# Optimization experiments

Hardware: AMD Instinct MI355X
Metric: run time of the kernel (lower is better)

Reference implementation:

```python
import jax, jax.numpy as jnp
import numpy as np
from jax import lax

B, CIN, T, H, W_ = 16, 8, 20, 64, 64
COUT = 32
K = 3


def setup_inputs() -> dict:
    key = jax.random.key(0)
    ks = jax.random.split(key, 6)
    scale = 0.05
    return {
        "X": jax.random.normal(ks[0], (B, CIN, T, H, W_), dtype=jnp.float32),
        "W": jax.random.normal(ks[1], (4 * COUT, CIN + COUT, K, K), dtype=jnp.float32) * scale,
        "b": jax.random.normal(ks[2], (4 * COUT,), dtype=jnp.float32) * scale,
        "W_ci": jax.random.normal(ks[3], (COUT, H, W_), dtype=jnp.float32) * scale,
        "W_cf": jax.random.normal(ks[4], (COUT, H, W_), dtype=jnp.float32) * scale,
        "W_co": jax.random.normal(ks[5], (COUT, H, W_), dtype=jnp.float32) * scale,
    }


def reference(X, W, b, W_ci, W_cf, W_co):
    # X: (B, Cin, T, H, W) -> output (B, Cout, T, H, W)
    Bb, Cin, Tt, Hh, Ww = X.shape
    Cout = W_ci.shape[0]

    def conv(x):  # x: (B, Cin+Cout, H, W)
        y = lax.conv_general_dilated(
            x, W, window_strides=(1, 1), padding="SAME",
            dimension_numbers=("NCHW", "OIHW", "NCHW"))
        return y + b[None, :, None, None]

    def step(carry, x_t):
        h, c = carry
        gates = conv(jnp.concatenate([x_t, h], axis=1))  # (B, 4*Cout, H, W)
        i_c, f_c, cc_c, o_c = jnp.split(gates, 4, axis=1)
        i_g = jax.nn.sigmoid(i_c + W_ci[None] * c)
        f_g = jax.nn.sigmoid(f_c + W_cf[None] * c)
        c_new = f_g * c + i_g * jnp.tanh(cc_c)
        o_g = jax.nn.sigmoid(o_c + W_co[None] * c_new)
        h_new = o_g * jnp.tanh(c_new)
        return (h_new, c_new), h_new

    h0 = jnp.zeros((Bb, Cout, Hh, Ww), dtype=X.dtype)
    c0 = jnp.zeros((Bb, Cout, Hh, Ww), dtype=X.dtype)
    x_seq = jnp.moveaxis(X, 2, 0)  # (T, B, Cin, H, W)
    _, hs = lax.scan(step, (h0, c0), x_seq)  # hs: (T, B, Cout, H, W)
    return jnp.moveaxis(hs, 0, 2)  # (B, Cout, T, H, W)
```

## Files before the change

### kernel.cpp

```cpp
#include <hip/hip_runtime.h>
#include <math.h>

#define Bn   16
#define CIN  8
#define NT   20
#define COUT 32
#define HW   4096
#define NTHREADS 256

typedef __attribute__((ext_vector_type(8)))  short bf16x8;
typedef __attribute__((ext_vector_type(16))) float f32x16;
typedef __attribute__((ext_vector_type(4)))  int   int4v;

__device__ inline unsigned short f2bf(float f) {
    unsigned u = __builtin_bit_cast(unsigned, f);
    u += 0x7fffu + ((u >> 16) & 1u);
    return (unsigned short)(u >> 16);
}
__device__ inline float bf2f(unsigned short u) {
    return __builtin_bit_cast(float, (unsigned)u << 16);
}
__device__ inline float sigm(float x) {
    return 1.0f / (1.0f + __expf(-x));
}
__device__ inline float tanh_fast(float x) {
    x = fminf(fmaxf(x, -15.0f), 15.0f);
    float e = __expf(2.0f * x);
    return (e - 1.0f) / (e + 1.0f);
}

__global__ __launch_bounds__(256) void prep_w(const float* __restrict__ W,
                                              unsigned short* __restrict__ Wbf) {
    int idx = blockIdx.x * 256 + threadIdx.x;
    if (idx >= 9 * 3 * 2 * 128 * 8) return;
    int e    = idx & 7;
    int m    = (idx >> 3) & 127;
    int half = (idx >> 10) & 1;
    int fk   = idx >> 11;
    int kb   = fk % 3;
    int tap  = fk / 3;
    int ch   = kb * 16 + half * 8 + e;
    int co   = m >> 2;
    int g    = m & 3;
    float v = 0.0f;
    if (ch < 40) v = W[(size_t)((g * 32 + co) * 40 + ch) * 9 + tap];
    Wbf[idx] = f2bf(v);
}

__global__ __launch_bounds__(256) void zero_flags(int* flags) {
    flags[blockIdx.x * 256 + threadIdx.x] = 0;
}

__global__ __launch_bounds__(NTHREADS, 2) void convlstm_persist(
    const float* __restrict__ X,
    const unsigned short* __restrict__ Wbf,
    const float* __restrict__ bias,
    const float* __restrict__ Wci,
    const float* __restrict__ Wcf,
    const float* __restrict__ Wco,
    float* __restrict__ out,
    unsigned long long* __restrict__ stage,
    int* __restrict__ flags)
{
    __shared__ __align__(16) unsigned char smem[33792 + 24576 + 512];
    unsigned short* Wlds = (unsigned short*)(smem + 33792);
    float*          lds_b = (float*)(smem + 33792 + 24576);

    const int tid = threadIdx.x;
    const int pid = blockIdx.x;
    const int b   = pid >> 5;
    const int TI  = ((pid & 7) << 2) | ((pid >> 3) & 3);
    const int r0  = TI * 2;

    const int wid  = tid >> 6;
    const int lane = tid & 63;
    const int lm   = lane & 31;
    const int half = lane >> 5;

    {
        int4v z = {0, 0, 0, 0};
        for (int i = tid; i < 2112; i += NTHREADS) *(int4v*)(smem + i * 16) = z;
    }
    {
        const float* wsrc[3] = {Wci, Wcf, Wco};
#pragma unroll
        for (int pl = 0; pl < 3; ++pl)
            for (int i = tid; i < 4096; i += NTHREADS) {
                int co = i >> 7, p = i & 127;
                Wlds[pl * 4096 + i] = f2bf(wsrc[pl][(co << 12) + TI * 128 + p]);
            }
        if (tid < 128) lds_b[tid] = bias[tid];
    }

    bf16x8 Af[27];
#pragma unroll
    for (int f = 0; f < 27; ++f)
        Af[f] = *(const bf16x8*)(Wbf + (size_t)((f * 2 + half) * 128 + wid * 32 + lm) * 8);

    float creg[16];
#pragma unroll
    for (int i = 0; i < 16; ++i) creg[i] = 0.0f;

    const unsigned sel0 = half ? 0x01000504u : 0x05040100u;
    const unsigned sel1 = sel0 + 0x02020202u;
    int* myflag = flags + (b << 5) + TI;

    const int  gr  = r0 + wid - 1;
    const bool rok = (unsigned)gr < 64u;
    const float* xbase = X + ((((size_t)b * CIN) * NT) << 12)
                           + (((rok ? gr : 0)) << 6) + lane;
    const size_t chs = (size_t)NT << 12;
    float xr[8];
    if (rok) {
#pragma unroll
        for (int k = 0; k < 8; ++k) xr[k] = xbase[(size_t)k * chs];
    }

    __syncthreads();

    for (int t = 0; t < NT; ++t) {
        const int lcF  = lane + 1;
        const int celF = wid * 33 + (lcF >> 1);
        const int sbF  = (lcF & 1) << 3;
        const int sxF  = (lcF >> 1) & 15;
        if (rok) {
            unsigned d0, d1, d2, d3;
            asm("v_cvt_pk_bf16_f32 %0, %1, %2" : "=v"(d0) : "v"(xr[0]), "v"(xr[1]));
            asm("v_cvt_pk_bf16_f32 %0, %1, %2" : "=v"(d1) : "v"(xr[2]), "v"(xr[3]));
            asm("v_cvt_pk_bf16_f32 %0, %1, %2" : "=v"(d2) : "v"(xr[4]), "v"(xr[5]));
            asm("v_cvt_pk_bf16_f32 %0, %1, %2" : "=v"(d3) : "v"(xr[6]), "v"(xr[7]));
            int4v xq = {(int)d0, (int)d1, (int)d2, (int)d3};
            *(int4v*)(smem + celF * 256 + ((sbF ^ sxF) << 4)) = xq;
        }
        const bool haloL = (wid == 0) && (TI > 0);
        const bool haloR = (wid == 3) && (TI < 31);
        if ((haloL || haloR) && t > 0) {
            if (lane == 0) {
                const int nti = haloL ? TI - 1 : TI + 1;
                const int* fp = flags + (b << 5) + nti;
                while (__hip_atomic_load(fp, __ATOMIC_RELAXED,
                                         __HIP_MEMORY_SCOPE_AGENT) < t)
                    __builtin_amdgcn_s_sleep(1);
            }
            const unsigned long long* sp =
                stage + ((((size_t)((t - 1) & 1) * Bn + b) * 64 + gr) << 9) + lane;
#pragma unroll
            for (int qq = 0; qq < 4; ++qq) {
                unsigned long long v0 = __hip_atomic_load(
                    sp + (2 * qq) * 64, __ATOMIC_RELAXED, __HIP_MEMORY_SCOPE_AGENT);
                unsigned long long v1 = __hip_atomic_load(
                    sp + (2 * qq + 1) * 64, __ATOMIC_RELAXED, __HIP_MEMORY_SCOPE_AGENT);
                const int slot = (sbF | (qq + 1)) ^ sxF;
                int4v hv = {(int)(unsigned)v0, (int)(v0 >> 32),
                            (int)(unsigned)v1, (int)(v1 >> 32)};
                *(int4v*)(smem + celF * 256 + (slot << 4)) = hv;
            }
        }
        __syncthreads();

        if (rok && t + 1 < NT) {
            const float* xp = xbase + ((size_t)(t + 1) << 12);
#pragma unroll
            for (int k = 0; k < 8; ++k) xr[k] = xp[(size_t)k * chs];
        }

        f32x16 acc[4];
#pragma unroll
        for (int nb = 0; nb < 4; ++nb)
#pragma unroll
            for (int r = 0; r < 16; ++r) acc[nb][r] = 0.0f;

        __builtin_amdgcn_s_setprio(1);
#pragma unroll
        for (int dy = 0; dy < 3; ++dy)
#pragma unroll
            for (int dx = 0; dx < 3; ++dx)
#pragma unroll
                for (int kb = 0; kb < 3; ++kb) {
                    const int f    = (dy * 3 + dx) * 3 + kb;
                    const int cidx = kb * 2 + half;
#pragma unroll
                    for (int nb = 0; nb < 4; ++nb) {
                        const int lr   = (nb >> 1) + dy;
                        const int lc   = lm + (nb & 1) * 32 + dx;
                        const int slot = (((lc & 1) << 3) + cidx) ^ ((lc >> 1) & 15);
                        const bf16x8 bf =
                            *(const bf16x8*)(smem + (lr * 33 + (lc >> 1)) * 256 + slot * 16);
                        acc[nb] = __builtin_amdgcn_mfma_f32_32x32x16_bf16(Af[f], bf, acc[nb], 0, 0, 0);
                    }
                }
        __builtin_amdgcn_s_setprio(0);

        __syncthreads();

#pragma unroll
        for (int nb = 0; nb < 4; ++nb) {
            const int p_loc = nb * 32 + lm;
            const int pos   = TI * 128 + p_loc;
            const int col   = (nb & 1) * 32 + lm;
            const int lc    = col + 1;
            const int cell  = (1 + (nb >> 1)) * 33 + (lc >> 1);
            const int sbase = (lc & 1) << 3;
            const int sx    = (lc >> 1) & 15;
            const int row   = r0 + (nb >> 1);
            const bool hstore = (nb >> 1) ? (TI < 31) : (TI > 0);
            float hprev = 0.0f;
#pragma unroll
            for (int j = 0; j < 4; ++j) {
                const int co  = wid * 8 + 2 * j + half;
                const int wof = (co << 7) + p_loc;
                const float c0 = creg[nb * 4 + j];
                const float gi = acc[nb][4 * j + 0] + lds_b[co]      + bf2f(Wlds[wof]) * c0;
                const float gf = acc[nb][4 * j + 1] + lds_b[32 + co] + bf2f(Wlds[4096 + wof]) * c0;
                const float gc = acc[nb][4 * j + 2] + lds_b[64 + co];
                const float gq = acc[nb][4 * j + 3] + lds_b[96 + co];

                const float ig = sigm(gi);
                const float fg = sigm(gf);
                const float cn = fg * c0 + ig * tanh_fast(gc);
                const float og = sigm(gq + bf2f(Wlds[2 * 4096 + wof]) * cn);
                const float hn = og * tanh_fast(cn);

                creg[nb * 4 + j] = cn;
                out[(((size_t)(b * COUT + co) * NT + t) << 12) + pos] = hn;

                if (j & 1) {
                    unsigned pk;
                    asm("v_cvt_pk_bf16_f32 %0, %1, %2" : "=v"(pk) : "v"(hprev), "v"(hn));
                    unsigned other = (unsigned)__shfl_xor((int)pk, 32, 64);
                    unsigned q0 = __builtin_amdgcn_perm(other, pk, sel0);
                    unsigned q1 = __builtin_amdgcn_perm(other, pk, sel1);
                    const int a = j >> 1;
                    if (half == a) {
                        const int q8 = wid * 2 + a;
                        const unsigned long long quad =
                            ((unsigned long long)q1 << 32) | q0;
                        const int tq = 2 + q8;
                        *(unsigned long long*)(smem + cell * 256 +
                            (((sbase | (tq >> 1)) ^ sx) << 4) + ((tq & 1) << 3)) = quad;
                        if (hstore)
                            __hip_atomic_store(
                                stage + ((((size_t)(t & 1) * Bn + b) * 64 + row) << 9)
                                      + (q8 << 6) + col,
                                quad, __ATOMIC_RELAXED, __HIP_MEMORY_SCOPE_AGENT);
                    }
                } else {
                    hprev = hn;
                }
            }
        }

        __syncthreads();
        if (tid == 0)
            __hip_atomic_store(myflag, t + 1, __ATOMIC_RELAXED,
                               __HIP_MEMORY_SCOPE_AGENT);
    }
}

extern "C" void kernel_launch(void* const* d_in, const int* in_sizes, int n_in,
                              void* d_out, int out_size, void* d_ws, size_t ws_size,
                              hipStream_t stream) {
    const float* X    = (const float*)d_in[0];
    const float* Wf   = (const float*)d_in[1];
    const float* bias = (const float*)d_in[2];
    const float* Wci  = (const float*)d_in[3];
    const float* Wcf  = (const float*)d_in[4];
    const float* Wco  = (const float*)d_in[5];
    float* out = (float*)d_out;

    unsigned short*     Wbf   = (unsigned short*)d_ws;
    int*                flags = (int*)((char*)d_ws + 110592);
    unsigned long long* stage = (unsigned long long*)((char*)d_ws + 112640);

    prep_w<<<216, 256, 0, stream>>>(Wf, Wbf);
    zero_flags<<<2, 256, 0, stream>>>(flags);
    convlstm_persist<<<Bn * 32, NTHREADS, 0, stream>>>(
        X, Wbf, bias, Wci, Wcf, Wco, out, stage, flags);
}
```

Before: 357.1 us.

## Fold bias into MFMA weights, stream weight fragments, and drop peephole LDS

The bias becomes a constant-one channel: the unused padded channel 40 at the centre tap holds the bias in the weight matrix, and the LDS halo is pre-filled with bf16 1.0 in that slot, so the bias add leaves the epilogue. The peephole weights are packed into one 64-bit global array per pixel and read directly instead of being staged in LDS. The 27 register-resident A fragments are replaced with per-dy loads from global memory, and the x prefetch is removed. Together these cut LDS and VGPR use so launch bounds can go from 2 to 3 blocks per SM. The cost is repeated global/L2 loads of weights every timestep, and x loads that are no longer hidden behind the MFMA loop.

```diff
diff --git a/kernel.cpp b/kernel.cpp
--- a/kernel.cpp
+++ b/kernel.cpp
@@ -30,6 +30,7 @@
 }
 
 __global__ __launch_bounds__(256) void prep_w(const float* __restrict__ W,
+                                              const float* __restrict__ bias,
                                               unsigned short* __restrict__ Wbf) {
     int idx = blockIdx.x * 256 + threadIdx.x;
     if (idx >= 9 * 3 * 2 * 128 * 8) return;
@@ -43,28 +44,35 @@
     int co   = m >> 2;
     int g    = m & 3;
     float v = 0.0f;
-    if (ch < 40) v = W[(size_t)((g * 32 + co) * 40 + ch) * 9 + tap];
+    if (ch < 40)                     v = W[(size_t)((g * 32 + co) * 40 + ch) * 9 + tap];
+    else if (ch == 40 && tap == 4)   v = bias[g * 32 + co];
     Wbf[idx] = f2bf(v);
+}
+
+__global__ __launch_bounds__(256) void prep_pk(const float* __restrict__ Wci,
+                                               const float* __restrict__ Wcf,
+                                               const float* __restrict__ Wco,
+                                               unsigned long long* __restrict__ Wpk) {
+    int idx = blockIdx.x * 256 + threadIdx.x;
+    unsigned long long v = (unsigned long long)f2bf(Wci[idx])
+                         | ((unsigned long long)f2bf(Wcf[idx]) << 16)
+                         | ((unsigned long long)f2bf(Wco[idx]) << 32);
+    Wpk[idx] = v;
 }
 
 __global__ __launch_bounds__(256) void zero_flags(int* flags) {
     flags[blockIdx.x * 256 + threadIdx.x] = 0;
 }
 
-__global__ __launch_bounds__(NTHREADS, 2) void convlstm_persist(
+__global__ __launch_bounds__(NTHREADS, 3) void convlstm_persist(
     const float* __restrict__ X,
     const unsigned short* __restrict__ Wbf,
-    const float* __restrict__ bias,
-    const float* __restrict__ Wci,
-    const float* __restrict__ Wcf,
-    const float* __restrict__ Wco,
+    const unsigned long long* __restrict__ Wpk,
     float* __restrict__ out,
     unsigned long long* __restrict__ stage,
     int* __restrict__ flags)
 {
-    __shared__ __align__(16) unsigned char smem[33792 + 24576 + 512];
-    unsigned short* Wlds = (unsigned short*)(smem + 33792);
-    float*          lds_b = (float*)(smem + 33792 + 24576);
+    __shared__ __align__(16) unsigned char smem[33792];
 
     const int tid = threadIdx.x;
     const int pid = blockIdx.x;
@@ -77,25 +85,16 @@
     const int lm   = lane & 31;
     const int half = lane >> 5;
 
-    {
-        int4v z = {0, 0, 0, 0};
-        for (int i = tid; i < 2112; i += NTHREADS) *(int4v*)(smem + i * 16) = z;
+    for (int id = tid; id < 2112; id += NTHREADS) {
+        const int cell  = id >> 4;
+        const int slot  = id & 15;
+        const int cp    = (cell % 33) & 15;
+        const int unswz = slot ^ cp;
+        int4v v = {((unswz & 7) == 5) ? 0x3F80 : 0, 0, 0, 0};
+        *(int4v*)(smem + cell * 256 + slot * 16) = v;
     }
-    {
-        const float* wsrc[3] = {Wci, Wcf, Wco};
-#pragma unroll
-        for (int pl = 0; pl < 3; ++pl)
-            for (int i = tid; i < 4096; i += NTHREADS) {
-                int co = i >> 7, p = i & 127;
-                Wlds[pl * 4096 + i] = f2bf(wsrc[pl][(co << 12) + TI * 128 + p]);
-            }
-        if (tid < 128) lds_b[tid] = bias[tid];
-    }
-
-    bf16x8 Af[27];
-#pragma unroll
-    for (int f = 0; f < 27; ++f)
-        Af[f] = *(const bf16x8*)(Wbf + (size_t)((f * 2 + half) * 128 + wid * 32 + lm) * 8);
+
+    const unsigned short* abase = Wbf + (size_t)(half * 128 + wid * 32 + lm) * 8;
 
     float creg[16];
 #pragma unroll
@@ -107,14 +106,6 @@
 
     const int  gr  = r0 + wid - 1;
     const bool rok = (unsigned)gr < 64u;
-    const float* xbase = X + ((((size_t)b * CIN) * NT) << 12)
-                           + (((rok ? gr : 0)) << 6) + lane;
-    const size_t chs = (size_t)NT << 12;
-    float xr[8];
-    if (rok) {
-#pragma unroll
-        for (int k = 0; k < 8; ++k) xr[k] = xbase[(size_t)k * chs];
-    }
 
     __syncthreads();
 
@@ -124,11 +115,15 @@
         const int sbF  = (lcF & 1) << 3;
         const int sxF  = (lcF >> 1) & 15;
         if (rok) {
+            const float* xp = X + ((((size_t)b * CIN) * NT + t) << 12) + (gr << 6) + lane;
+            const size_t chs = (size_t)NT << 12;
+            float x0 = xp[0],       x1 = xp[chs],     x2 = xp[2 * chs], x3 = xp[3 * chs];
+            float x4 = xp[4 * chs], x5 = xp[5 * chs], x6 = xp[6 * chs], x7 = xp[7 * chs];
             unsigned d0, d1, d2, d3;
-            asm("v_cvt_pk_bf16_f32 %0, %1, %2" : "=v"(d0) : "v"(xr[0]), "v"(xr[1]));
-            asm("v_cvt_pk_bf16_f32 %0, %1, %2" : "=v"(d1) : "v"(xr[2]), "v"(xr[3]));
-            asm("v_cvt_pk_bf16_f32 %0, %1, %2" : "=v"(d2) : "v"(xr[4]), "v"(xr[5]));
-            asm("v_cvt_pk_bf16_f32 %0, %1, %2" : "=v"(d3) : "v"(xr[6]), "v"(xr[7]));
+            asm("v_cvt_pk_bf16_f32 %0, %1, %2" : "=v"(d0) : "v"(x0), "v"(x1));
+            asm("v_cvt_pk_bf16_f32 %0, %1, %2" : "=v"(d1) : "v"(x2), "v"(x3));
+            asm("v_cvt_pk_bf16_f32 %0, %1, %2" : "=v"(d2) : "v"(x4), "v"(x5));
+            asm("v_cvt_pk_bf16_f32 %0, %1, %2" : "=v"(d3) : "v"(x6), "v"(x7));
             int4v xq = {(int)d0, (int)d1, (int)d2, (int)d3};
             *(int4v*)(smem + celF * 256 + ((sbF ^ sxF) << 4)) = xq;
         }
@@ -158,12 +153,6 @@
         }
         __syncthreads();
 
-        if (rok && t + 1 < NT) {
-            const float* xp = xbase + ((size_t)(t + 1) << 12);
-#pragma unroll
-            for (int k = 0; k < 8; ++k) xr[k] = xp[(size_t)k * chs];
-        }
-
         f32x16 acc[4];
 #pragma unroll
         for (int nb = 0; nb < 4; ++nb)
@@ -172,12 +161,15 @@
 
         __builtin_amdgcn_s_setprio(1);
 #pragma unroll
-        for (int dy = 0; dy < 3; ++dy)
+        for (int dy = 0; dy < 3; ++dy) {
+            bf16x8 a[9];
+#pragma unroll
+            for (int i = 0; i < 9; ++i)
+                a[i] = *(const bf16x8*)(abase + (size_t)(dy * 9 + i) * 2048);
 #pragma unroll
             for (int dx = 0; dx < 3; ++dx)
 #pragma unroll
                 for (int kb = 0; kb < 3; ++kb) {
-                    const int f    = (dy * 3 + dx) * 3 + kb;
                     const int cidx = kb * 2 + half;
 #pragma unroll
                     for (int nb = 0; nb < 4; ++nb) {
@@ -186,9 +178,11 @@
                         const int slot = (((lc & 1) << 3) + cidx) ^ ((lc >> 1) & 15);
                         const bf16x8 bf =
                             *(const bf16x8*)(smem + (lr * 33 + (lc >> 1)) * 256 + slot * 16);
-                        acc[nb] = __builtin_amdgcn_mfma_f32_32x32x16_bf16(Af[f], bf, acc[nb], 0, 0, 0);
+                        acc[nb] = __builtin_amdgcn_mfma_f32_32x32x16_bf16(
+                            a[dx * 3 + kb], bf, acc[nb], 0, 0, 0);
                     }
                 }
+        }
         __builtin_amdgcn_s_setprio(0);
 
         __syncthreads();
@@ -207,18 +201,22 @@
             float hprev = 0.0f;
 #pragma unroll
             for (int j = 0; j < 4; ++j) {
-                const int co  = wid * 8 + 2 * j + half;
-                const int wof = (co << 7) + p_loc;
+                const int co = wid * 8 + 2 * j + half;
+                const unsigned long long wp = Wpk[(co << 12) + pos];
+                const float wci = bf2f((unsigned short)wp);
+                const float wcf = bf2f((unsigned short)(wp >> 16));
+                const float wco = bf2f((unsigned short)(wp >> 32));
+
                 const float c0 = creg[nb * 4 + j];
-                const float gi = acc[nb][4 * j + 0] + lds_b[co]      + bf2f(Wlds[wof]) * c0;
-                const float gf = acc[nb][4 * j + 1] + lds_b[32 + co] + bf2f(Wlds[4096 + wof]) * c0;
-                const float gc = acc[nb][4 * j + 2] + lds_b[64 + co];
-                const float gq = acc[nb][4 * j + 3] + lds_b[96 + co];
+                const float gi = acc[nb][4 * j + 0] + wci * c0;
+                const float gf = acc[nb][4 * j + 1] + wcf * c0;
+                const float gc = acc[nb][4 * j + 2];
+                const float gq = acc[nb][4 * j + 3];
 
                 const float ig = sigm(gi);
                 const float fg = sigm(gf);
                 const float cn = fg * c0 + ig * tanh_fast(gc);
-                const float og = sigm(gq + bf2f(Wlds[2 * 4096 + wof]) * cn);
+                const float og = sigm(gq + wco * cn);
                 const float hn = og * tanh_fast(cn);
 
                 creg[nb * 4 + j] = cn;
@@ -269,11 +267,13 @@
     float* out = (float*)d_out;
 
     unsigned short*     Wbf   = (unsigned short*)d_ws;
-    int*                flags = (int*)((char*)d_ws + 110592);
-    unsigned long long* stage = (unsigned long long*)((char*)d_ws + 112640);
-
-    prep_w<<<216, 256, 0, stream>>>(Wf, Wbf);
+    unsigned long long* Wpk   = (unsigned long long*)((char*)d_ws + 110592);
+    int*                flags = (int*)((char*)d_ws + 110592 + 1048576);
+    unsigned long long* stage = (unsigned long long*)((char*)d_ws + 110592 + 1048576 + 2048);
+
+    prep_w<<<216, 256, 0, stream>>>(Wf, bias, Wbf);
+    prep_pk<<<512, 256, 0, stream>>>(Wci, Wcf, Wco, Wpk);
     zero_flags<<<2, 256, 0, stream>>>(flags);
     convlstm_persist<<<Bn * 32, NTHREADS, 0, stream>>>(
-        X, Wbf, bias, Wci, Wcf, Wco, out, stage, flags);
-}
+        X, Wbf, Wpk, out, stage, flags);
+}
```

Measured after the change: 607.8 us. 70.2% more time.

## Double-buffer x input in LDS and write next step during epilogue

Applied to the files above, without the earlier changes.

The x_t tile is now written into one of two alternating LDS slots (slots 6/7) during the previous step's epilogue, instead of at the start of each step before the barrier. The first MFMA K-block for the even half selects the current slot by parity of t. This shortens the critical path between the flag wait and the convolution and drops the register-held xr prefetch, though the global load now sits right before the gate epilogue. It depends on the LDS slots 6/7 being otherwise unused.

```diff
diff --git a/kernel.cpp b/kernel.cpp
--- a/kernel.cpp
+++ b/kernel.cpp
@@ -105,33 +105,30 @@
     const unsigned sel1 = sel0 + 0x02020202u;
     int* myflag = flags + (b << 5) + TI;
 
-    const int  gr  = r0 + wid - 1;
-    const bool rok = (unsigned)gr < 64u;
-    const float* xbase = X + ((((size_t)b * CIN) * NT) << 12)
-                           + (((rok ? gr : 0)) << 6) + lane;
+    const int  gr   = r0 + wid - 1;
+    const bool rok  = (unsigned)gr < 64u;
+    const int  lcF  = lane + 1;
+    const int  celF = wid * 33 + (lcF >> 1);
+    const int  sbF  = (lcF & 1) << 3;
+    const int  sxF  = (lcF >> 1) & 15;
     const size_t chs = (size_t)NT << 12;
-    float xr[8];
+
     if (rok) {
-#pragma unroll
-        for (int k = 0; k < 8; ++k) xr[k] = xbase[(size_t)k * chs];
+        const float* xp = X + ((((size_t)b * CIN) * NT) << 12) + (gr << 6) + lane;
+        float x0 = xp[0],       x1 = xp[chs],     x2 = xp[2 * chs], x3 = xp[3 * chs];
+        float x4 = xp[4 * chs], x5 = xp[5 * chs], x6 = xp[6 * chs], x7 = xp[7 * chs];
+        unsigned d0, d1, d2, d3;
+        asm("v_cvt_pk_bf16_f32 %0, %1, %2" : "=v"(d0) : "v"(x0), "v"(x1));
+        asm("v_cvt_pk_bf16_f32 %0, %1, %2" : "=v"(d1) : "v"(x2), "v"(x3));
+        asm("v_cvt_pk_bf16_f32 %0, %1, %2" : "=v"(d2) : "v"(x4), "v"(x5));
+        asm("v_cvt_pk_bf16_f32 %0, %1, %2" : "=v"(d3) : "v"(x6), "v"(x7));
+        int4v xq = {(int)d0, (int)d1, (int)d2, (int)d3};
+        *(int4v*)(smem + celF * 256 + (((sbF | 6) ^ sxF) << 4)) = xq;
     }
 
     __syncthreads();
 
     for (int t = 0; t < NT; ++t) {
-        const int lcF  = lane + 1;
-        const int celF = wid * 33 + (lcF >> 1);
-        const int sbF  = (lcF & 1) << 3;
-        const int sxF  = (lcF >> 1) & 15;
-        if (rok) {
-            unsigned d0, d1, d2, d3;
-            asm("v_cvt_pk_bf16_f32 %0, %1, %2" : "=v"(d0) : "v"(xr[0]), "v"(xr[1]));
-            asm("v_cvt_pk_bf16_f32 %0, %1, %2" : "=v"(d1) : "v"(xr[2]), "v"(xr[3]));
-            asm("v_cvt_pk_bf16_f32 %0, %1, %2" : "=v"(d2) : "v"(xr[4]), "v"(xr[5]));
-            asm("v_cvt_pk_bf16_f32 %0, %1, %2" : "=v"(d3) : "v"(xr[6]), "v"(xr[7]));
-            int4v xq = {(int)d0, (int)d1, (int)d2, (int)d3};
-            *(int4v*)(smem + celF * 256 + ((sbF ^ sxF) << 4)) = xq;
-        }
         const bool haloL = (wid == 0) && (TI > 0);
         const bool haloR = (wid == 3) && (TI < 31);
         if ((haloL || haloR) && t > 0) {
@@ -158,12 +155,7 @@
         }
         __syncthreads();
 
-        if (rok && t + 1 < NT) {
-            const float* xp = xbase + ((size_t)(t + 1) << 12);
-#pragma unroll
-            for (int k = 0; k < 8; ++k) xr[k] = xp[(size_t)k * chs];
-        }
-
+        const int cidx0 = half ? 1 : (6 + (t & 1));
         f32x16 acc[4];
 #pragma unroll
         for (int nb = 0; nb < 4; ++nb)
@@ -178,7 +170,7 @@
 #pragma unroll
                 for (int kb = 0; kb < 3; ++kb) {
                     const int f    = (dy * 3 + dx) * 3 + kb;
-                    const int cidx = kb * 2 + half;
+                    const int cidx = (kb == 0) ? cidx0 : (kb * 2 + half);
 #pragma unroll
                     for (int nb = 0; nb < 4; ++nb) {
                         const int lr   = (nb >> 1) + dy;
@@ -192,6 +184,15 @@
         __builtin_amdgcn_s_setprio(0);
 
         __syncthreads();
+
+        float xn[8];
+        const bool xok = rok && (t + 1 < NT);
+        if (xok) {
+            const float* xp = X + ((((size_t)b * CIN) * NT + (t + 1)) << 12)
+                                + (gr << 6) + lane;
+#pragma unroll
+            for (int k = 0; k < 8; ++k) xn[k] = xp[(size_t)k * chs];
+        }
 
 #pragma unroll
         for (int nb = 0; nb < 4; ++nb) {
@@ -250,6 +251,16 @@
             }
         }
 
+        if (xok) {
+            unsigned d0, d1, d2, d3;
+            asm("v_cvt_pk_bf16_f32 %0, %1, %2" : "=v"(d0) : "v"(xn[0]), "v"(xn[1]));
+            asm("v_cvt_pk_bf16_f32 %0, %1, %2" : "=v"(d1) : "v"(xn[2]), "v"(xn[3]));
+            asm("v_cvt_pk_bf16_f32 %0, %1, %2" : "=v"(d2) : "v"(xn[4]), "v"(xn[5]));
+            asm("v_cvt_pk_bf16_f32 %0, %1, %2" : "=v"(d3) : "v"(xn[6]), "v"(xn[7]));
+            int4v xq = {(int)d0, (int)d1, (int)d2, (int)d3};
+            *(int4v*)(smem + celF * 256 + (((sbF | (7 - (t & 1))) ^ sxF) << 4)) = xq;
+        }
+
         __syncthreads();
         if (tid == 0)
             __hip_atomic_store(myflag, t + 1, __ATOMIC_RELAXED,
```

New measurement: 417.3 us. 1.17x slower.

## Replace block barrier before flag with per-wave flag increments and deferred stores

Applied to the files above, without the earlier changes.

Each wave now publishes its halo h values to the staging buffer and then atomically increments the tile flag once the stage stores retire (vmcnt wait). The end-of-step __syncthreads is dropped, and neighbours wait for the flag to reach 4*t. Output stores are deferred until after the stage stores so they do not delay the flag, and the X prefetch into registers is replaced by direct loads at the start of each step. Barriers now use an explicit lgkmcnt wait instead of a full waitcnt. Risks include a weaker ordering guarantee on the relaxed flag protocol and exposed X load latency.

```diff
diff --git a/kernel.cpp b/kernel.cpp
--- a/kernel.cpp
+++ b/kernel.cpp
@@ -27,6 +27,12 @@
     x = fminf(fmaxf(x, -15.0f), 15.0f);
     float e = __expf(2.0f * x);
     return (e - 1.0f) / (e + 1.0f);
+}
+
+__device__ inline void barrier_lgkm() {
+    asm volatile("s_waitcnt lgkmcnt(0)" ::: "memory");
+    __builtin_amdgcn_s_barrier();
+    asm volatile("" ::: "memory");
 }
 
 __global__ __launch_bounds__(256) void prep_w(const float* __restrict__ W,
@@ -107,14 +113,7 @@
 
     const int  gr  = r0 + wid - 1;
     const bool rok = (unsigned)gr < 64u;
-    const float* xbase = X + ((((size_t)b * CIN) * NT) << 12)
-                           + (((rok ? gr : 0)) << 6) + lane;
     const size_t chs = (size_t)NT << 12;
-    float xr[8];
-    if (rok) {
-#pragma unroll
-        for (int k = 0; k < 8; ++k) xr[k] = xbase[(size_t)k * chs];
-    }
 
     __syncthreads();
 
@@ -124,11 +123,14 @@
         const int sbF  = (lcF & 1) << 3;
         const int sxF  = (lcF >> 1) & 15;
         if (rok) {
+            const float* xp = X + ((((size_t)b * CIN) * NT + t) << 12) + (gr << 6) + lane;
+            float x0 = xp[0],       x1 = xp[chs],     x2 = xp[2 * chs], x3 = xp[3 * chs];
+            float x4 = xp[4 * chs], x5 = xp[5 * chs], x6 = xp[6 * chs], x7 = xp[7 * chs];
             unsigned d0, d1, d2, d3;
-            asm("v_cvt_pk_bf16_f32 %0, %1, %2" : "=v"(d0) : "v"(xr[0]), "v"(xr[1]));
-            asm("v_cvt_pk_bf16_f32 %0, %1, %2" : "=v"(d1) : "v"(xr[2]), "v"(xr[3]));
-            asm("v_cvt_pk_bf16_f32 %0, %1, %2" : "=v"(d2) : "v"(xr[4]), "v"(xr[5]));
-            asm("v_cvt_pk_bf16_f32 %0, %1, %2" : "=v"(d3) : "v"(xr[6]), "v"(xr[7]));
+            asm("v_cvt_pk_bf16_f32 %0, %1, %2" : "=v"(d0) : "v"(x0), "v"(x1));
+            asm("v_cvt_pk_bf16_f32 %0, %1, %2" : "=v"(d1) : "v"(x2), "v"(x3));
+            asm("v_cvt_pk_bf16_f32 %0, %1, %2" : "=v"(d2) : "v"(x4), "v"(x5));
+            asm("v_cvt_pk_bf16_f32 %0, %1, %2" : "=v"(d3) : "v"(x6), "v"(x7));
             int4v xq = {(int)d0, (int)d1, (int)d2, (int)d3};
             *(int4v*)(smem + celF * 256 + ((sbF ^ sxF) << 4)) = xq;
         }
@@ -139,7 +141,7 @@
                 const int nti = haloL ? TI - 1 : TI + 1;
                 const int* fp = flags + (b << 5) + nti;
                 while (__hip_atomic_load(fp, __ATOMIC_RELAXED,
-                                         __HIP_MEMORY_SCOPE_AGENT) < t)
+                                         __HIP_MEMORY_SCOPE_AGENT) < 4 * t)
                     __builtin_amdgcn_s_sleep(1);
             }
             const unsigned long long* sp =
@@ -156,13 +158,7 @@
                 *(int4v*)(smem + celF * 256 + (slot << 4)) = hv;
             }
         }
-        __syncthreads();
-
-        if (rok && t + 1 < NT) {
-            const float* xp = xbase + ((size_t)(t + 1) << 12);
-#pragma unroll
-            for (int k = 0; k < 8; ++k) xr[k] = xp[(size_t)k * chs];
-        }
+        barrier_lgkm();
 
         f32x16 acc[4];
 #pragma unroll
@@ -191,19 +187,17 @@
                 }
         __builtin_amdgcn_s_setprio(0);
 
-        __syncthreads();
-
+        barrier_lgkm();
+
+        unsigned long long qr[4];
 #pragma unroll
         for (int nb = 0; nb < 4; ++nb) {
             const int p_loc = nb * 32 + lm;
-            const int pos   = TI * 128 + p_loc;
             const int col   = (nb & 1) * 32 + lm;
             const int lc    = col + 1;
             const int cell  = (1 + (nb >> 1)) * 33 + (lc >> 1);
             const int sbase = (lc & 1) << 3;
             const int sx    = (lc >> 1) & 15;
-            const int row   = r0 + (nb >> 1);
-            const bool hstore = (nb >> 1) ? (TI < 31) : (TI > 0);
             float hprev = 0.0f;
 #pragma unroll
             for (int j = 0; j < 4; ++j) {
@@ -222,7 +216,7 @@
                 const float hn = og * tanh_fast(cn);
 
                 creg[nb * 4 + j] = cn;
-                out[(((size_t)(b * COUT + co) * NT + t) << 12) + pos] = hn;
+                acc[nb][4 * j + 3] = hn;
 
                 if (j & 1) {
                     unsigned pk;
@@ -238,11 +232,7 @@
                         const int tq = 2 + q8;
                         *(unsigned long long*)(smem + cell * 256 +
                             (((sbase | (tq >> 1)) ^ sx) << 4) + ((tq & 1) << 3)) = quad;
-                        if (hstore)
-                            __hip_atomic_store(
-                                stage + ((((size_t)(t & 1) * Bn + b) * 64 + row) << 9)
-                                      + (q8 << 6) + col,
-                                quad, __ATOMIC_RELAXED, __HIP_MEMORY_SCOPE_AGENT);
+                        qr[nb] = quad;
                     }
                 } else {
                     hprev = hn;
@@ -250,10 +240,33 @@
             }
         }
 
-        __syncthreads();
-        if (tid == 0)
-            __hip_atomic_store(myflag, t + 1, __ATOMIC_RELAXED,
-                               __HIP_MEMORY_SCOPE_AGENT);
+        {
+            const int q8 = wid * 2 + half;
+#pragma unroll
+            for (int nb = 0; nb < 4; ++nb) {
+                const int row = r0 + (nb >> 1);
+                const int col = (nb & 1) * 32 + lm;
+                __hip_atomic_store(
+                    stage + ((((size_t)(t & 1) * Bn + b) * 64 + row) << 9)
+                          + (q8 << 6) + col,
+                    qr[nb], __ATOMIC_RELAXED, __HIP_MEMORY_SCOPE_AGENT);
+            }
+        }
+        asm volatile("" ::: "memory");
+#pragma unroll
+        for (int nb = 0; nb < 4; ++nb) {
+            const int pos = TI * 128 + nb * 32 + lm;
+#pragma unroll
+            for (int j = 0; j < 4; ++j) {
+                const int co = wid * 8 + 2 * j + half;
+                out[(((size_t)(b * COUT + co) * NT + t) << 12) + pos] = acc[nb][4 * j + 3];
+            }
+        }
+        asm volatile("s_waitcnt vmcnt(16)" ::: "memory");
+        __builtin_amdgcn_sched_barrier(0);
+        if (lane == 0)
+            __hip_atomic_fetch_add(myflag, 1, __ATOMIC_RELAXED,
+                                   __HIP_MEMORY_SCOPE_AGENT);
     }
 }
 
```

New measurement: 350.5 us. Within noise of the previous version (-1.8%).
